# Kernel tuning notes

Hardware: AMD Instinct MI355X
Metric: run time of the kernel (lower is better)

The kernel has to match this reference:

```python
import jax, jax.numpy as jnp
import numpy as np

B, N_DET, N_T, NY, NX = 8, 128, 2048, 256, 256


def setup_inputs() -> dict:
    key = jax.random.key(0)
    k1, k2, k3 = jax.random.split(key, 3)
    sino = jax.random.normal(k1, (B, 1, N_DET, N_T), dtype=jnp.float32)
    # LUT channel 0: fractional time index (some out-of-range to exercise valid mask)
    lut0 = jax.random.uniform(k2, (NY, NX, N_DET), dtype=jnp.float32,
                              minval=-8.0, maxval=float(N_T) + 8.0)
    alpha = jax.random.uniform(k3, (NY, NX, N_DET), dtype=jnp.float32)
    k_floor = jnp.floor(lut0)
    valid = (k_floor >= 0) & (k_floor < N_T - 1)
    k0 = jnp.clip(k_floor, 0, N_T - 2).astype(jnp.int32)
    # Hann apodization window over detectors
    win = 0.5 - 0.5 * np.cos(2.0 * np.pi * np.arange(N_DET) / max(N_DET - 1, 1))
    apod = jnp.asarray(win.astype(np.float32))
    return {"sino": sino, "alpha": alpha, "apod": apod, "k0": k0, "valid": valid}


def reference(sino, alpha, apod, k0, valid):
    # Per-sample normalization over (n_det, n_t)
    eps = jnp.finfo(sino.dtype).eps
    mean = jnp.mean(sino, axis=(-1, -2), keepdims=True)
    centered = sino - mean
    std = jnp.sqrt(jnp.mean(centered * centered, axis=(-1, -2), keepdims=True) + eps)
    S = (centered / std)[:, 0]                     # [B, n_det, n_t]

    P = NY * NX
    kd = jnp.transpose(k0, (2, 0, 1)).reshape(N_DET, P)      # [n_det, P]
    ad = jnp.transpose(alpha, (2, 0, 1)).reshape(N_DET, P)   # [n_det, P]
    vd = jnp.transpose(valid, (2, 0, 1)).reshape(N_DET, P).astype(S.dtype)

    idx0 = jnp.broadcast_to(kd[None], (B, N_DET, P))
    s0 = jnp.take_along_axis(S, idx0, axis=2)                # [B, n_det, P]
    s1 = jnp.take_along_axis(S, idx0 + 1, axis=2)            # [B, n_det, P]
    sk = ((1.0 - ad) * s0 + ad * s1) * vd                    # linear interp + mask

    out = jnp.einsum('d,bdp->bp', apod, sk).reshape(B, NY, NX)
    norm = jnp.maximum(jnp.sum(apod), jnp.finfo(apod.dtype).tiny)
    return (out / norm)[:, None]                             # [B, 1, ny, nx]
```

## Files before the change

### kernel.cpp

```cpp
#include <hip/hip_runtime.h>
#include <hip/hip_fp16.h>

#define NB    8
#define NDET  128
#define NT    2048
#define NPIX  65536
#define NELEM (NDET * NT)
#define NGRP  32


#define WS_S16_OFF   8192
#define WS_PT_OFF    (8192 + (size_t)NDET * NT * NB * 2)
#define WS3_REQUIRED (WS_PT_OFF + (size_t)NGRP * NPIX * NB * 2)
#define WS2_REQUIRED (WS_PT_OFF + (size_t)8 * NB * NPIX * 4)

__global__ __launch_bounds__(256) void k_stats(const float* __restrict__ sino,
                                               double* __restrict__ wsd) {
    const int bx = blockIdx.x;
    const int b = bx >> 5, i = bx & 31;
    const float4* src = (const float4*)(sino + (size_t)b * NELEM);
    const int base = i * 2048;
    double s = 0.0, ss = 0.0;
    for (int r = 0; r < 8; ++r) {
        float4 v = src[base + r * 256 + threadIdx.x];
        double d0 = v.x, d1 = v.y, d2 = v.z, d3 = v.w;
        s  += d0 + d1 + d2 + d3;
        ss += d0 * d0 + d1 * d1 + d2 * d2 + d3 * d3;
    }
    for (int off = 32; off; off >>= 1) {
        s  += __shfl_down(s, off);
        ss += __shfl_down(ss, off);
    }
    __shared__ double lds[8];
    const int wave = threadIdx.x >> 6;
    if ((threadIdx.x & 63) == 0) { lds[wave * 2] = s; lds[wave * 2 + 1] = ss; }
    __syncthreads();
    if (threadIdx.x == 0) {
        double S = 0, SS = 0;
        for (int w = 0; w < 4; ++w) { S += lds[w * 2]; SS += lds[w * 2 + 1]; }
        wsd[bx * 2] = S; wsd[bx * 2 + 1] = SS;
    }
}

__global__ __launch_bounds__(256) void k_finalize(const float* __restrict__ apod,
                                                  const unsigned char* __restrict__ validb,
                                                  const double* __restrict__ wsd,
                                                  float* __restrict__ wsf) {
    __shared__ float sap[NDET];
    __shared__ int sflag;
    const int t = threadIdx.x;
    if (t == 0) sflag = 0;
    if (t < NDET) sap[t] = apod[t];
    int local = 0;
    {
        const unsigned char* vb = validb + t * 256;
        for (int j = 1; j < 256; j += 4) local |= (vb[j] != 0);
    }
    __syncthreads();
    if (local) atomicOr(&sflag, 1);
    if (t < NB) {
        double S = 0, SS = 0;
        for (int i = 0; i < 32; ++i) {
            S  += wsd[(t * 32 + i) * 2];
            SS += wsd[(t * 32 + i) * 2 + 1];
        }
        double mean = S / (double)NELEM;
        double var  = SS / (double)NELEM - mean * mean;
        double istd = 1.0 / sqrt(var + (double)(1.1920928955078125e-07f));
        wsf[t]     = (float)mean;
        wsf[8 + t] = (float)istd;
    }
    if (t == 0) {
        double a = 0;
        for (int d = 0; d < NDET; ++d) a += (double)sap[d];
        float norm = fmaxf((float)a, 1.1754943508222875e-38f);
        wsf[17] = 1.0f / norm;
    }
    __syncthreads();
    if (t < NDET) wsf[32 + t] = sap[t] * wsf[17];
    if (t == 0) ((unsigned int*)wsf)[16] = (unsigned int)(sflag != 0);
}

__global__ __launch_bounds__(256) void k_build(const float* __restrict__ sino,
                                               const float* __restrict__ wsf,
                                               __half* __restrict__ S16) {
    const int dt = blockIdx.x * 256 + threadIdx.x;
    union { uint4 q; __half h[8]; } u;
#pragma unroll
    for (int b = 0; b < NB; ++b) {
        float x = sino[(size_t)b * NELEM + dt];
        u.h[b] = __float2half((x - wsf[b]) * wsf[8 + b]);
    }
    *(uint4*)(S16 + (size_t)dt * 8) = u.q;
}

__device__ __forceinline__ float2 h2f(unsigned int w) {
    __half2 h;
    *reinterpret_cast<unsigned int*>(&h) = w;
    return __half22float2(h);
}

__global__ __launch_bounds__(1024) void k_das4(const int* __restrict__ k0,
                                               const float* __restrict__ alpha,
                                               const void* __restrict__ valid,
                                               const __half* __restrict__ S16,
                                               const float* __restrict__ wsf,
                                               __half* __restrict__ pT) {
    __shared__ __align__(16) __half SL[4 * NT * NB];
    const int x     = blockIdx.x & 7;
    const int sub   = (blockIdx.x >> 3) & 3;
    const int chunk = blockIdx.x >> 5;
    const int g     = x * 4 + sub;
    {
        const uint4* src = (const uint4*)(S16 + (size_t)g * 4 * NT * NB);
        uint4* dst = (uint4*)SL;
#pragma unroll
        for (int i = 0; i < 8; ++i)
            dst[i * 1024 + threadIdx.x] = src[i * 1024 + threadIdx.x];
    }
    __syncthreads();

    const int lane = threadIdx.x & 63;
    const int wave = threadIdx.x >> 6;
    const int dl   = lane & 3;
    const int d    = g * 4 + dl;
    const int pxo  = lane >> 2;
    const unsigned int mode = ((const unsigned int*)wsf)[16];
    const float apn = wsf[32 + d];

    const int p0 = chunk * 8192 + wave * 16 + pxo;
    size_t li = (size_t)p0 * NDET + d;

    int          k_n = k0[li];
    float        a_n = alpha[li];
    unsigned int v_n = mode ? (unsigned int)((const unsigned char*)valid)[li]
                            : ((const unsigned int*)valid)[li];

    for (int it = 0; it < 32; ++it) {
        const int          kk = k_n;
        const float        aa = a_n;
        const unsigned int vv = v_n;
        const size_t lin = li + (it < 31 ? (size_t)256 * NDET : 0);
        k_n = k0[lin];
        a_n = alpha[lin];
        v_n = mode ? (unsigned int)((const unsigned char*)valid)[lin]
                   : ((const unsigned int*)valid)[lin];

        const float w  = vv ? apn : 0.0f;
        const float wb = w * aa;
        const float wa = w - wb;
        const uint4* s = (const uint4*)(SL + ((size_t)(dl * NT + kk) << 3));
        uint4 q0 = s[0];
        uint4 q1 = s[1];
        float acc[NB];
        {
            const unsigned int w0[4] = {q0.x, q0.y, q0.z, q0.w};
            const unsigned int w1[4] = {q1.x, q1.y, q1.z, q1.w};
#pragma unroll
            for (int h = 0; h < 4; ++h) {
                float2 f0 = h2f(w0[h]);
                float2 f1 = h2f(w1[h]);
                acc[2 * h]     = wa * f0.x + wb * f1.x;
                acc[2 * h + 1] = wa * f0.y + wb * f1.y;
            }
        }
#pragma unroll
        for (int b = 0; b < NB; ++b) {
            acc[b] += __shfl_xor(acc[b], 1);
            acc[b] += __shfl_xor(acc[b], 2);
        }
        if (dl == 0) {
            union { uint4 q; __half2 h[4]; } o;
#pragma unroll
            for (int h = 0; h < 4; ++h)
                o.h[h] = __floats2half2_rn(acc[2 * h], acc[2 * h + 1]);
            const int p = p0 + it * 256;
            *(uint4*)(pT + ((size_t)g * NPIX + p) * NB) = o.q;
        }
        li += (size_t)256 * NDET;
    }
}

__global__ __launch_bounds__(256) void k_reduce2(const __half* __restrict__ pT,
                                                 float* __restrict__ out) {
    const int p = blockIdx.x * 256 + threadIdx.x;
    float acc[NB] = {0.f, 0.f, 0.f, 0.f, 0.f, 0.f, 0.f, 0.f};
#pragma unroll
    for (int g = 0; g < NGRP; ++g) {
        union { uint4 q; __half2 h[4]; } u;
        u.q = *(const uint4*)(pT + ((size_t)g * NPIX + p) * NB);
#pragma unroll
        for (int h = 0; h < 4; ++h) {
            float2 f = __half22float2(u.h[h]);
            acc[2 * h]     += f.x;
            acc[2 * h + 1] += f.y;
        }
    }
#pragma unroll
    for (int b = 0; b < NB; ++b)
        out[(size_t)b * NPIX + p] = acc[b];
}

__global__ __launch_bounds__(1024) void k_das2(const int* __restrict__ k0,
                                               const float* __restrict__ alpha,
                                               const void* __restrict__ valid,
                                               const __half* __restrict__ S16,
                                               const float* __restrict__ wsf,
                                               float* __restrict__ partials) {
    const int px = threadIdx.x & 255;
    const int dc = threadIdx.x >> 8;
    const int slice = blockIdx.x & 7;
    const int chunk = blockIdx.x >> 3;
    const int p  = chunk * 256 + px;
    const int d0 = slice * 16 + dc * 4;
    const unsigned int mode = ((const unsigned int*)wsf)[16];
    const float* apodn = wsf + 32;

    float acc[NB] = {0.f, 0.f, 0.f, 0.f, 0.f, 0.f, 0.f, 0.f};
    const size_t lbase = (size_t)p * NDET + d0;

    int4   k4 = *(const int4*)(k0 + lbase);
    float4 a4 = *(const float4*)(alpha + lbase);
    unsigned int vbits;
    if (mode) {
        unsigned int v4 = *(const unsigned int*)((const unsigned char*)valid + lbase);
        vbits = ((v4 & 0xffu) ? 1u : 0u) | (((v4 >> 8) & 0xffu) ? 2u : 0u) |
                (((v4 >> 16) & 0xffu) ? 4u : 0u) | ((v4 >> 24) ? 8u : 0u);
    } else {
        uint4 v4 = *(const uint4*)((const unsigned int*)valid + lbase);
        vbits = (v4.x ? 1u : 0u) | (v4.y ? 2u : 0u) | (v4.z ? 4u : 0u) | (v4.w ? 8u : 0u);
    }
    const int   kk[4] = {k4.x, k4.y, k4.z, k4.w};
    const float aa[4] = {a4.x, a4.y, a4.z, a4.w};
#pragma unroll
    for (int j = 0; j < 4; ++j) {
        const int d = d0 + j;
        const float w  = ((vbits >> j) & 1u) ? apodn[d] : 0.0f;
        const float wb = w * aa[j];
        const float wa = w - wb;
        const uint4* s = (const uint4*)(S16 + ((size_t)(d * NT + kk[j]) << 3));
        uint4 q0 = s[0];
        uint4 q1 = s[1];
        const unsigned int w0[4] = {q0.x, q0.y, q0.z, q0.w};
        const unsigned int w1[4] = {q1.x, q1.y, q1.z, q1.w};
#pragma unroll
        for (int h = 0; h < 4; ++h) {
            float2 f0 = h2f(w0[h]);
            float2 f1 = h2f(w1[h]);
            acc[2 * h]     += wa * f0.x + wb * f1.x;
            acc[2 * h + 1] += wa * f0.y + wb * f1.y;
        }
    }

    __shared__ float red[1024][9];
#pragma unroll
    for (int b = 0; b < NB; ++b) red[threadIdx.x][b] = acc[b];
    __syncthreads();
    if (dc == 0) {
#pragma unroll
        for (int b = 0; b < NB; ++b) {
            float v = red[px][b] + red[px + 256][b] + red[px + 512][b] + red[px + 768][b];
            partials[((size_t)slice * NB + b) * NPIX + p] = v;
        }
    }
}

__global__ __launch_bounds__(256) void k_reduce(const float* __restrict__ partials,
                                                float* __restrict__ out) {
    const int i = (blockIdx.x * 256 + threadIdx.x) * 4;
    float4 s = {0.f, 0.f, 0.f, 0.f};
#pragma unroll
    for (int g = 0; g < 8; ++g) {
        float4 v = *(const float4*)(partials + (size_t)g * NB * NPIX + i);
        s.x += v.x; s.y += v.y; s.z += v.z; s.w += v.w;
    }
    *(float4*)(out + i) = s;
}

extern "C" void kernel_launch(void* const* d_in, const int* in_sizes, int n_in,
                              void* d_out, int out_size, void* d_ws, size_t ws_size,
                              hipStream_t stream) {
    const float* sino  = (const float*)d_in[0];
    const float* alpha = (const float*)d_in[1];
    const float* apod  = (const float*)d_in[2];
    const int*   k0    = (const int*)d_in[3];
    const void*  valid = d_in[4];

    float*  out = (float*)d_out;
    double* wsd = (double*)d_ws;
    float*  wsf = (float*)((char*)d_ws + 4096);
    __half* S16 = (__half*)((char*)d_ws + WS_S16_OFF);
    __half* pT  = (__half*)((char*)d_ws + WS_PT_OFF);
    float*  parts = (float*)((char*)d_ws + WS_PT_OFF);

    k_stats   <<<256,  256, 0, stream>>>(sino, wsd);
    k_finalize<<<1,    256, 0, stream>>>(apod, (const unsigned char*)valid, wsd, wsf);
    k_build   <<<1024, 256, 0, stream>>>(sino, wsf, S16);
    if (ws_size >= WS3_REQUIRED) {
        k_das4   <<<256, 1024, 0, stream>>>(k0, alpha, valid, S16, wsf, pT);
        k_reduce2<<<256,  256, 0, stream>>>(pT, out);
    } else {
        k_das2  <<<2048, 1024, 0, stream>>>(k0, alpha, valid, S16, wsf, parts);
        k_reduce<<<512,   256, 0, stream>>>(parts, out);
    }
}
```

Baseline: 75.89 us.

## Assign one pixel per thread over four detectors with vectorized LUT loads

The DAS kernel is remapped so each thread handles one pixel across all four detectors of its group, rather than four lanes splitting detectors and combining through cross-lane shuffles. LUT, alpha and valid entries are now fetched as 16-byte (or 4-byte for byte masks) vector loads, and the shuffle reduction is gone. Each thread also writes a full output every iteration instead of one lane in four. In exchange, per-thread register use goes up and LDS gathers from the four detector rows happen inside one thread, which may raise bank conflicts.

After: 72.73 us. 4.2% less time.

```diff
diff --git a/kernel.cpp b/kernel.cpp
--- a/kernel.cpp
+++ b/kernel.cpp
@@ -100,7 +100,7 @@
     return __half22float2(h);
 }
 
-__global__ __launch_bounds__(1024) void k_das4(const int* __restrict__ k0,
+__global__ __launch_bounds__(1024) void k_das5(const int* __restrict__ k0,
                                                const float* __restrict__ alpha,
                                                const void* __restrict__ valid,
                                                const __half* __restrict__ S16,
@@ -120,64 +120,68 @@
     }
     __syncthreads();
 
-    const int lane = threadIdx.x & 63;
-    const int wave = threadIdx.x >> 6;
-    const int dl   = lane & 3;
-    const int d    = g * 4 + dl;
-    const int pxo  = lane >> 2;
     const unsigned int mode = ((const unsigned int*)wsf)[16];
-    const float apn = wsf[32 + d];
-
-    const int p0 = chunk * 8192 + wave * 16 + pxo;
-    size_t li = (size_t)p0 * NDET + d;
-
-    int          k_n = k0[li];
-    float        a_n = alpha[li];
-    unsigned int v_n = mode ? (unsigned int)((const unsigned char*)valid)[li]
-                            : ((const unsigned int*)valid)[li];
-
-    for (int it = 0; it < 32; ++it) {
-        const int          kk = k_n;
-        const float        aa = a_n;
-        const unsigned int vv = v_n;
-        const size_t lin = li + (it < 31 ? (size_t)256 * NDET : 0);
-        k_n = k0[lin];
-        a_n = alpha[lin];
-        v_n = mode ? (unsigned int)((const unsigned char*)valid)[lin]
-                   : ((const unsigned int*)valid)[lin];
-
-        const float w  = vv ? apn : 0.0f;
-        const float wb = w * aa;
-        const float wa = w - wb;
-        const uint4* s = (const uint4*)(SL + ((size_t)(dl * NT + kk) << 3));
-        uint4 q0 = s[0];
-        uint4 q1 = s[1];
-        float acc[NB];
-        {
+    float apn[4];
+#pragma unroll
+    for (int j = 0; j < 4; ++j) apn[j] = wsf[32 + g * 4 + j];
+
+    const int p0 = chunk * 8192 + (int)threadIdx.x;
+    size_t li = (size_t)p0 * NDET + g * 4;
+
+    int4         kb = *(const int4*)(k0 + li);
+    float4       ab = *(const float4*)(alpha + li);
+    unsigned int vB = 0;
+    uint4        vW = {0u, 0u, 0u, 0u};
+    if (mode) vB = *(const unsigned int*)((const unsigned char*)valid + li);
+    else      vW = *(const uint4*)((const unsigned int*)valid + li);
+
+    for (int it = 0; it < 8; ++it) {
+        const int4         kc = kb;
+        const float4       ac = ab;
+        const unsigned int cB = vB;
+        const uint4        cW = vW;
+        if (it < 7) {
+            const size_t lin = li + (size_t)1024 * NDET;
+            kb = *(const int4*)(k0 + lin);
+            ab = *(const float4*)(alpha + lin);
+            if (mode) vB = *(const unsigned int*)((const unsigned char*)valid + lin);
+            else      vW = *(const uint4*)((const unsigned int*)valid + lin);
+        }
+        unsigned int vbits;
+        if (mode)
+            vbits = ((cB & 0xffu) ? 1u : 0u) | ((cB & 0xff00u) ? 2u : 0u) |
+                    ((cB & 0xff0000u) ? 4u : 0u) | ((cB & 0xff000000u) ? 8u : 0u);
+        else
+            vbits = (cW.x ? 1u : 0u) | (cW.y ? 2u : 0u) | (cW.z ? 4u : 0u) | (cW.w ? 8u : 0u);
+
+        const int   kk[4] = {kc.x, kc.y, kc.z, kc.w};
+        const float aa[4] = {ac.x, ac.y, ac.z, ac.w};
+        float acc[NB] = {0.f, 0.f, 0.f, 0.f, 0.f, 0.f, 0.f, 0.f};
+#pragma unroll
+        for (int j = 0; j < 4; ++j) {
+            const float w  = ((vbits >> j) & 1u) ? apn[j] : 0.0f;
+            const float wb = w * aa[j];
+            const float wa = w - wb;
+            const uint4* s = (const uint4*)(SL + ((size_t)(j * NT + kk[j]) << 3));
+            uint4 q0 = s[0];
+            uint4 q1 = s[1];
             const unsigned int w0[4] = {q0.x, q0.y, q0.z, q0.w};
             const unsigned int w1[4] = {q1.x, q1.y, q1.z, q1.w};
 #pragma unroll
             for (int h = 0; h < 4; ++h) {
                 float2 f0 = h2f(w0[h]);
                 float2 f1 = h2f(w1[h]);
-                acc[2 * h]     = wa * f0.x + wb * f1.x;
-                acc[2 * h + 1] = wa * f0.y + wb * f1.y;
+                acc[2 * h]     += wa * f0.x + wb * f1.x;
+                acc[2 * h + 1] += wa * f0.y + wb * f1.y;
             }
         }
-#pragma unroll
-        for (int b = 0; b < NB; ++b) {
-            acc[b] += __shfl_xor(acc[b], 1);
-            acc[b] += __shfl_xor(acc[b], 2);
-        }
-        if (dl == 0) {
-            union { uint4 q; __half2 h[4]; } o;
-#pragma unroll
-            for (int h = 0; h < 4; ++h)
-                o.h[h] = __floats2half2_rn(acc[2 * h], acc[2 * h + 1]);
-            const int p = p0 + it * 256;
-            *(uint4*)(pT + ((size_t)g * NPIX + p) * NB) = o.q;
-        }
-        li += (size_t)256 * NDET;
+        union { uint4 q; __half2 h[4]; } o;
+#pragma unroll
+        for (int h = 0; h < 4; ++h)
+            o.h[h] = __floats2half2_rn(acc[2 * h], acc[2 * h + 1]);
+        const int p = p0 + it * 1024;
+        *(uint4*)(pT + ((size_t)g * NPIX + p) * NB) = o.q;
+        li += (size_t)1024 * NDET;
     }
 }
 
@@ -297,7 +301,7 @@
     k_finalize<<<1,    256, 0, stream>>>(apod, (const unsigned char*)valid, wsd, wsf);
     k_build   <<<1024, 256, 0, stream>>>(sino, wsf, S16);
     if (ws_size >= WS3_REQUIRED) {
-        k_das4   <<<256, 1024, 0, stream>>>(k0, alpha, valid, S16, wsf, pT);
+        k_das5   <<<256, 1024, 0, stream>>>(k0, alpha, valid, S16, wsf, pT);
         k_reduce2<<<256,  256, 0, stream>>>(pT, out);
     } else {
         k_das2  <<<2048, 1024, 0, stream>>>(k0, alpha, valid, S16, wsf, parts);
```
